# Kernel tuning notes

Measured on AMD Instinct MI355X. Metric: run time of the kernel, lower is better.

The kernel has to match this reference:

```python
import jax, jax.numpy as jnp
import numpy as np

# cfg dims: B batch, LQ max_que_len, O max_opt_count, LO max_opt_len,
# S max_sent_para, W max_words_sent, D word_emb
B, LQ, O, LO, S, W, D = 64, 64, 8, 32, 64, 32, 512
NEG_BIG = -9.0e15  # torch masked_fill constant for empty sentences


def setup_inputs() -> dict:
    key = jax.random.key(0)
    k1, k2, k3 = jax.random.split(key, 3)
    que_feat = jax.random.normal(k1, (B, LQ, D), dtype=jnp.float32)
    opt_feat = jax.random.normal(k2, (B, O, LO, D), dtype=jnp.float32)
    csf = jax.random.normal(k3, (B, S, W, D), dtype=jnp.float32)
    csf_mask = jnp.zeros((B, S, W), dtype=bool)   # True = padding word
    opt_sum = jnp.zeros((B, O), dtype=bool)       # True = empty option
    return dict(que_feat=que_feat, opt_feat=opt_feat, csf=csf,
                csf_mask=csf_mask, opt_sum=opt_sum)


def reference(que_feat, opt_feat, csf, csf_mask, opt_sum):
    b, s, w, d = csf.shape
    o = opt_feat.shape[1]

    # per-sentence valid length; empty sentences get a huge-magnitude divisor
    csf_len = jnp.sum(~csf_mask, axis=-1)                      # [B,S]
    csf_len = jnp.where(csf_len == 0, NEG_BIG,
                        csf_len.astype(jnp.float32))

    # question -> context sentence score: sum over query words and sentence
    # words of dot products (original: matmul + two sums, fused here)
    att_q2c = jnp.einsum('bqd,bswd->bs', que_feat, csf)        # [B,S]
    ix_q2c = jnp.argmax(att_q2c / csf_len, axis=-1)            # [B]

    # gather best sentence per batch item, broadcast over options
    que_csf = jnp.take_along_axis(
        csf, ix_q2c[:, None, None, None], axis=1)[:, 0]        # [B,W,D]
    que_csf = jnp.broadcast_to(que_csf[:, None], (b, o, w, d))
    que_csf = jnp.where(opt_sum[:, :, None, None], 0.0, que_csf)

    # option -> context sentence score
    att_o2c = jnp.einsum('bold,bswd->bos', opt_feat, csf)      # [B,O,S]
    ix_o2c = jnp.argmax(att_o2c / csf_len[:, None, :], axis=-1)  # [B,O]

    # faithful to original get_opt2csf: indexes csf[0] for EVERY batch item
    opt_csf = csf[0][ix_o2c]                                   # [B,O,W,D]
    opt_csf = jnp.where(opt_sum[:, :, None, None], 0.0, opt_csf)

    # make_mask: positions whose feature vector is all-zero
    que_csf_mask = jnp.sum(jnp.abs(que_csf), axis=-1) == 0     # [B,O,W]
    opt_csf_mask = jnp.sum(jnp.abs(opt_csf), axis=-1) == 0     # [B,O,W]
    return que_csf, que_csf_mask, opt_csf, opt_csf_mask
```

## Files before the change

### kernel.cpp

```cpp
#include <hip/hip_runtime.h>
#include <hip/hip_cooperative_groups.h>
#include <stddef.h>

namespace cg = cooperative_groups;

#define B  64
#define LQ 64
#define O  8
#define LO 32
#define S  64
#define W  32
#define D  512

#define NEG_BIG (-9.0e15f)

#define QUE_CSF_SZ  (B*O*W*D)
#define MASK_SZ     (B*O*W)
#define OFF_QMASK   (QUE_CSF_SZ)
#define OFF_OPT     (QUE_CSF_SZ + MASK_SZ)
#define OFF_OMASK   (QUE_CSF_SZ + MASK_SZ + QUE_CSF_SZ)

#define WS_QSUMH 0
#define WS_OSUM  (B*2*D)
#define WS_SC    (B*2*D + B*O*D)

#define NBLK 2368

using f4 = __attribute__((ext_vector_type(4))) float;

__device__ inline float dot4(f4 a, f4 b) {
  return a.x * b.x + a.y * b.y + a.z * b.z + a.w * b.w;
}

#define RED(v)                \
  do {                        \
    v += __shfl_xor(v, 32);   \
    v += __shfl_xor(v, 16);   \
    v += __shfl_xor(v, 8);    \
    v += __shfl_xor(v, 4);    \
    v += __shfl_xor(v, 2);    \
    v += __shfl_xor(v, 1);    \
  } while (0)

#define ARGMAX(v, idx)                                         \
  do {                                                         \
    for (int off_ = 32; off_; off_ >>= 1) {                    \
      float ov_ = __shfl_xor(v, off_);                         \
      int oi_ = __shfl_xor(idx, off_);                         \
      if (ov_ > v || (ov_ == v && oi_ < idx)) { v = ov_; idx = oi_; } \
    }                                                          \
  } while (0)

__device__ inline void dots9(const float* __restrict__ ws, f4 acc, int b,
                             int wv, int lane, float part[2][9]) {
  const f4* qh = (const f4*)(ws + WS_QSUMH) + (size_t)b * 256;
  const int t = wv * 64 + lane;
  f4 qs = qh[t] + qh[128 + t];
  float pq = dot4(acc, qs);
  float po[O];
  #pragma unroll
  for (int o = 0; o < O; ++o)
    po[o] = dot4(acc, ((const f4*)(ws + WS_OSUM))[((size_t)(b * O + o)) * 128 + t]);
  RED(pq);
  #pragma unroll
  for (int o = 0; o < O; ++o) RED(po[o]);
  if (lane == 0) {
    part[wv][0] = pq;
    #pragma unroll
    for (int o = 0; o < O; ++o) part[wv][1 + o] = po[o];
  }
}

__global__ __launch_bounds__(128, 5) void k_fused(
    const float* __restrict__ que, const float* __restrict__ opt,
    const float* __restrict__ csf, const unsigned char* __restrict__ csf_mask,
    const unsigned char* __restrict__ opt_sum, float* __restrict__ ws,
    float* __restrict__ out) {
  const int blk = blockIdx.x;
  const int t = threadIdx.x;
  const int wv = t >> 6;
  const int lane = t & 63;
  const int g1 = blk + NBLK;
  const bool j1csf = (g1 < 4096);

  const f4* p0 = (const f4*)csf + (size_t)blk * 4096 + t;
  const f4* p1;
  if (j1csf)            p1 = (const f4*)csf + (size_t)g1 * 4096 + t;
  else if (g1 < 4224)   p1 = (const f4*)que + (size_t)(g1 - 4096) * 4096 + t;
  else                  p1 = (const f4*)opt + (size_t)(g1 - 4224) * 4096 + t;

  f4 acc0 = {0.f, 0.f, 0.f, 0.f};
  f4 acc1 = {0.f, 0.f, 0.f, 0.f};
  #pragma unroll 8
  for (int r = 0; r < 32; ++r) {
    acc0 += p0[(size_t)r * 128];
    acc1 += p1[(size_t)r * 128];
  }
  if (!j1csf) {
    if (g1 < 4224)
      ((f4*)(ws + WS_QSUMH))[(size_t)(g1 - 4096) * 128 + t] = acc1;
    else
      ((f4*)(ws + WS_OSUM))[(size_t)(g1 - 4224) * 128 + t] = acc1;
  }

  __threadfence();
  cg::this_grid().sync();

  __shared__ float part[2][2][9];
  dots9(ws, acc0, blk >> 6, wv, lane, part[0]);
  if (j1csf) dots9(ws, acc1, g1 >> 6, wv, lane, part[1]);

  float len;
  {
    const int bs = (wv == 0) ? blk : g1;
    int pad = 0;
    if (lane < W && (wv == 0 || j1csf))
      pad = (csf_mask[(size_t)bs * W + lane] != 0) ? 1 : 0;
    const unsigned long long bal = __ballot(pad);
    const int valid = W - (int)__popcll(bal);
    len = (valid == 0) ? NEG_BIG : (float)valid;
  }
  __syncthreads();

  if (t < 9) {
    const int b0 = blk >> 6, s0 = blk & 63;
    ws[WS_SC + ((size_t)t * B + b0) * S + s0] =
        (part[0][0][t] + part[0][1][t]) / len;
  }
  if (j1csf && t >= 64 && t < 73) {
    const int q = t - 64;
    const int b1 = g1 >> 6, s1 = g1 & 63;
    ws[WS_SC + ((size_t)q * B + b1) * S + s1] =
        (part[1][0][q] + part[1][1][q]) / len;
  }

  __threadfence();
  cg::this_grid().sync();

  for (int row = blk * 2 + wv; row < B * O * W; row += NBLK * 2) {
    const int w = row & 31;
    const int bo = row >> 5;
    const int b = bo >> 3;
    const int o = bo & 7;

    float vq_ = ws[WS_SC + (size_t)b * S + lane];
    int iq = lane;
    ARGMAX(vq_, iq);
    float vo_ = ws[WS_SC + ((size_t)(1 + o) * B + b) * S + lane];
    int io = lane;
    ARGMAX(vo_, io);

    const bool zero = (opt_sum[bo] != 0);
    f4 a0 = {0.f, 0.f, 0.f, 0.f}, a1 = a0, b0 = a0, b1 = a0;
    if (!zero) {
      const f4* qrow = (const f4*)csf + (((size_t)b * S + iq) * W + w) * 128;
      a0 = qrow[lane];
      a1 = qrow[64 + lane];
      const f4* orow = (const f4*)csf + ((size_t)io * W + w) * 128;
      b0 = orow[lane];
      b1 = orow[64 + lane];
    }
    f4* oq = (f4*)(out + (size_t)row * D);
    f4* oo = (f4*)(out + OFF_OPT + (size_t)row * D);
    __builtin_nontemporal_store(a0, oq + lane);
    __builtin_nontemporal_store(a1, oq + 64 + lane);
    __builtin_nontemporal_store(b0, oo + lane);
    __builtin_nontemporal_store(b1, oo + 64 + lane);

    float aq = fabsf(a0.x) + fabsf(a0.y) + fabsf(a0.z) + fabsf(a0.w) +
               fabsf(a1.x) + fabsf(a1.y) + fabsf(a1.z) + fabsf(a1.w);
    float ao = fabsf(b0.x) + fabsf(b0.y) + fabsf(b0.z) + fabsf(b0.w) +
               fabsf(b1.x) + fabsf(b1.y) + fabsf(b1.z) + fabsf(b1.w);
    RED(aq);
    RED(ao);
    if (lane == 0) {
      out[OFF_QMASK + row] = (aq == 0.f) ? 1.f : 0.f;
      out[OFF_OMASK + row] = (ao == 0.f) ? 1.f : 0.f;
    }
  }
}

template <int ROWS>
__device__ inline void rowsum4(const f4* __restrict__ src, f4* __restrict__ dst,
                               int t) {
  const int quarter = t >> 7;
  const int col = t & 127;
  const f4* p = src + (size_t)(quarter * (ROWS / 4)) * 128 + col;
  f4 acc = {0.f, 0.f, 0.f, 0.f};
  #pragma unroll
  for (int r = 0; r < ROWS / 4; ++r) acc += p[(size_t)r * 128];
  __shared__ f4 tmp[3][128];
  if (quarter) tmp[quarter - 1][col] = acc;
  __syncthreads();
  if (quarter == 0) dst[col] = acc + tmp[0][col] + tmp[1][col] + tmp[2][col];
}

__global__ __launch_bounds__(512) void k_qosum(
    const float* __restrict__ que, const float* __restrict__ opt,
    float* __restrict__ ws) {
  const int blk = blockIdx.x;
  const int t = threadIdx.x;
  if (blk < B) {
    rowsum4<LQ>((const f4*)que + (size_t)blk * LQ * 128,
                (f4*)(ws + WS_QSUMH) + (size_t)blk * 256, t);
    if (t < 128) {
      f4 z = {0.f, 0.f, 0.f, 0.f};
      ((f4*)(ws + WS_QSUMH))[(size_t)blk * 256 + 128 + t] = z;
    }
  } else {
    const int bo = blk - B;
    rowsum4<LO>((const f4*)opt + (size_t)bo * LO * 128,
                (f4*)(ws + WS_OSUM) + (size_t)bo * 128, t);
  }
}

__global__ __launch_bounds__(128) void k_score(
    const float* __restrict__ csf, const unsigned char* __restrict__ csf_mask,
    float* __restrict__ ws) {
  const int bs = blockIdx.x;
  const int b = bs >> 6;
  const int s = bs & 63;
  const int t = threadIdx.x;
  const int wv = t >> 6;
  const int lane = t & 63;

  const f4* p = (const f4*)csf + (size_t)bs * 4096 + t;
  f4 acc = {0.f, 0.f, 0.f, 0.f};
  #pragma unroll 8
  for (int r = 0; r < 32; ++r) acc += p[(size_t)r * 128];

  __shared__ float part[2][9];
  dots9(ws, acc, b, wv, lane, part);

  int pad = 0;
  if (lane < W) pad = (csf_mask[(size_t)bs * W + lane] != 0) ? 1 : 0;
  const unsigned long long bal = __ballot(pad);
  const int valid = W - (int)__popcll(bal);
  const float len = (valid == 0) ? NEG_BIG : (float)valid;

  __syncthreads();
  if (t < 9)
    ws[WS_SC + ((size_t)t * B + b) * S + s] = (part[0][t] + part[1][t]) / len;
}

__global__ __launch_bounds__(128) void k_gather(
    const float* __restrict__ csf, const unsigned char* __restrict__ opt_sum,
    const float* __restrict__ ws, float* __restrict__ out) {
  const int bow = blockIdx.x;
  const int w = bow & 31;
  const int bo = bow >> 5;
  const int b = bo >> 3;
  const int o = bo & 7;
  const int t = threadIdx.x;
  const int wv = t >> 6;
  const int lane = t & 63;

  __shared__ int sh_ix[2];
  {
    const int q = (wv == 0) ? 0 : (1 + o);
    float v = ws[WS_SC + ((size_t)q * B + b) * S + lane];
    int idx = lane;
    ARGMAX(v, idx);
    if (lane == 0) sh_ix[wv] = idx;
  }
  __syncthreads();

  const bool zero = (opt_sum[bo] != 0);
  f4 vq = {0.f, 0.f, 0.f, 0.f};
  f4 vo = {0.f, 0.f, 0.f, 0.f};
  if (!zero) {
    const int iq = sh_ix[0];
    const int io = sh_ix[1];
    vq = ((const f4*)csf)[(((size_t)b * S + iq) * W + w) * 128 + t];
    vo = ((const f4*)csf)[((size_t)io * W + w) * 128 + t];
  }
  __builtin_nontemporal_store(vq, (f4*)(out + (size_t)bow * D) + t);
  __builtin_nontemporal_store(vo, (f4*)(out + OFF_OPT + (size_t)bow * D) + t);

  float aq = fabsf(vq.x) + fabsf(vq.y) + fabsf(vq.z) + fabsf(vq.w);
  float ao = fabsf(vo.x) + fabsf(vo.y) + fabsf(vo.z) + fabsf(vo.w);
  RED(aq);
  RED(ao);

  __shared__ float sq[2], so[2];
  if (lane == 0) { sq[wv] = aq; so[wv] = ao; }
  __syncthreads();
  if (t == 0) {
    out[OFF_QMASK + bow] = ((sq[0] + sq[1]) == 0.f) ? 1.f : 0.f;
    out[OFF_OMASK + bow] = ((so[0] + so[1]) == 0.f) ? 1.f : 0.f;
  }
}

extern "C" void kernel_launch(void* const* d_in, const int* in_sizes, int n_in,
                              void* d_out, int out_size, void* d_ws, size_t ws_size,
                              hipStream_t stream) {
  const float* que = (const float*)d_in[0];
  const float* opt = (const float*)d_in[1];
  const float* csf = (const float*)d_in[2];
  const unsigned char* csf_mask = (const unsigned char*)d_in[3];
  const unsigned char* opt_sum = (const unsigned char*)d_in[4];
  float* out = (float*)d_out;
  float* ws = (float*)d_ws;

  int coop = 0;
  {
    int dev = 0;
    hipDeviceProp_t prop{};
    int mb = 0;
    if (hipGetDevice(&dev) == hipSuccess &&
        hipGetDeviceProperties(&prop, dev) == hipSuccess &&
        hipOccupancyMaxActiveBlocksPerMultiprocessor(&mb, k_fused, 128, 0) ==
            hipSuccess) {
      if (prop.cooperativeLaunch &&
          (long)mb * prop.multiProcessorCount >= NBLK)
        coop = 1;
    }
  }

  if (coop) {
    void* args[] = {(void*)&que, (void*)&opt, (void*)&csf, (void*)&csf_mask,
                    (void*)&opt_sum, (void*)&ws, (void*)&out};
    if (hipLaunchCooperativeKernel(k_fused, dim3(NBLK), dim3(128), args, 0,
                                   stream) != hipSuccess)
      coop = 0;
  }
  if (!coop) {
    k_qosum<<<B + B * O, 512, 0, stream>>>(que, opt, ws);
    k_score<<<B * S, 128, 0, stream>>>(csf, csf_mask, ws);
    k_gather<<<B * O * W, 128, 0, stream>>>(csf, opt_sum, ws, out);
  }
}
```

Measured before the change: 70.59 us.

## Replace cooperative grid syncs with atomic-flag pipeline and dynamic chunk scheduling

Drops the cooperative launch and its two grid-wide barriers in favour of a regular launch of 2048 blocks. Blocks first compute the question and option sums and signal a counter, then pull sentence chunks from an atomic work queue, computing scores and bumping per-batch done counters. Each block then spins only on its own batch's counter before gathering 8 output rows. The intent is to overlap phases and replace full-grid barriers with finer-grained dependencies. It relies on all 2048 blocks being co-resident (assumes 256 CUs from the occupancy check), adds a memset launch, and risks deadlock or spin contention if residency fails.

```diff
diff --git a/kernel.cpp b/kernel.cpp
--- a/kernel.cpp
+++ b/kernel.cpp
@@ -1,8 +1,5 @@
 #include <hip/hip_runtime.h>
-#include <hip/hip_cooperative_groups.h>
 #include <stddef.h>
-
-namespace cg = cooperative_groups;
 
 #define B  64
 #define LQ 64
@@ -23,8 +20,12 @@
 #define WS_QSUMH 0
 #define WS_OSUM  (B*2*D)
 #define WS_SC    (B*2*D + B*O*D)
-
-#define NBLK 2368
+#define WS_FLAGS (WS_SC + 9*B*S)
+#define N_FLAGS  66
+
+#define NBLK      2048
+#define N_SUM     640
+#define N_CSF     4096
 
 using f4 = __attribute__((ext_vector_type(4))) float;
 
@@ -42,14 +43,21 @@
     v += __shfl_xor(v, 1);    \
   } while (0)
 
-#define ARGMAX(v, idx)                                         \
-  do {                                                         \
-    for (int off_ = 32; off_; off_ >>= 1) {                    \
-      float ov_ = __shfl_xor(v, off_);                         \
-      int oi_ = __shfl_xor(idx, off_);                         \
+#define ARGMAX(v, idx)                                                \
+  do {                                                                \
+    for (int off_ = 32; off_; off_ >>= 1) {                           \
+      float ov_ = __shfl_xor(v, off_);                                \
+      int oi_ = __shfl_xor(idx, off_);                                \
       if (ov_ > v || (ov_ == v && oi_ < idx)) { v = ov_; idx = oi_; } \
-    }                                                          \
+    }                                                                 \
   } while (0)
+
+__device__ inline f4 stream32(const f4* __restrict__ p, int t) {
+  f4 acc = {0.f, 0.f, 0.f, 0.f};
+  #pragma unroll 8
+  for (int r = 0; r < 32; ++r) acc += p[(size_t)r * 128 + t];
+  return acc;
+}
 
 __device__ inline void dots9(const float* __restrict__ ws, f4 acc, int b,
                              int wv, int lane, float part[2][9]) {
@@ -71,7 +79,17 @@
   }
 }
 
-__global__ __launch_bounds__(128, 5) void k_fused(
+__device__ inline void spin_until(int* p, int target) {
+  if (threadIdx.x == 0) {
+    while (__hip_atomic_load(p, __ATOMIC_ACQUIRE, __HIP_MEMORY_SCOPE_AGENT) <
+           target)
+      __builtin_amdgcn_s_sleep(8);
+  }
+  __syncthreads();
+  __threadfence();
+}
+
+__global__ __launch_bounds__(128, 4) void k_pipe(
     const float* __restrict__ que, const float* __restrict__ opt,
     const float* __restrict__ csf, const unsigned char* __restrict__ csf_mask,
     const unsigned char* __restrict__ opt_sum, float* __restrict__ ws,
@@ -80,68 +98,73 @@
   const int t = threadIdx.x;
   const int wv = t >> 6;
   const int lane = t & 63;
-  const int g1 = blk + NBLK;
-  const bool j1csf = (g1 < 4096);
-
-  const f4* p0 = (const f4*)csf + (size_t)blk * 4096 + t;
-  const f4* p1;
-  if (j1csf)            p1 = (const f4*)csf + (size_t)g1 * 4096 + t;
-  else if (g1 < 4224)   p1 = (const f4*)que + (size_t)(g1 - 4096) * 4096 + t;
-  else                  p1 = (const f4*)opt + (size_t)(g1 - 4224) * 4096 + t;
-
-  f4 acc0 = {0.f, 0.f, 0.f, 0.f};
-  f4 acc1 = {0.f, 0.f, 0.f, 0.f};
-  #pragma unroll 8
-  for (int r = 0; r < 32; ++r) {
-    acc0 += p0[(size_t)r * 128];
-    acc1 += p1[(size_t)r * 128];
-  }
-  if (!j1csf) {
-    if (g1 < 4224)
-      ((f4*)(ws + WS_QSUMH))[(size_t)(g1 - 4096) * 128 + t] = acc1;
-    else
-      ((f4*)(ws + WS_OSUM))[(size_t)(g1 - 4224) * 128 + t] = acc1;
-  }
-
-  __threadfence();
-  cg::this_grid().sync();
-
-  __shared__ float part[2][2][9];
-  dots9(ws, acc0, blk >> 6, wv, lane, part[0]);
-  if (j1csf) dots9(ws, acc1, g1 >> 6, wv, lane, part[1]);
-
-  float len;
-  {
-    const int bs = (wv == 0) ? blk : g1;
+
+  int* flags = (int*)(ws + WS_FLAGS);
+  int* done_sum = flags;
+  int* next_chunk = flags + 1;
+  int* done_score = flags + 2;
+
+  if (blk < N_SUM) {
+    f4 acc;
+    if (blk < 128) {
+      acc = stream32((const f4*)que + (size_t)blk * 4096, t);
+      ((f4*)(ws + WS_QSUMH))[(size_t)blk * 128 + t] = acc;
+    } else {
+      const int bo = blk - 128;
+      acc = stream32((const f4*)opt + (size_t)bo * 4096, t);
+      ((f4*)(ws + WS_OSUM))[(size_t)bo * 128 + t] = acc;
+    }
+    __syncthreads();
+    if (t == 0) {
+      __threadfence();
+      __hip_atomic_fetch_add(done_sum, 1, __ATOMIC_RELEASE,
+                             __HIP_MEMORY_SCOPE_AGENT);
+    }
+  }
+
+  __shared__ int sh_c;
+  __shared__ float part[2][9];
+  bool waited = false;
+  for (;;) {
+    if (t == 0) sh_c = atomicAdd(next_chunk, 1);
+    __syncthreads();
+    const int c = sh_c;
+    __syncthreads();
+    if (c >= N_CSF) break;
+    const int b = c >> 6, s = c & 63;
+
+    f4 acc = stream32((const f4*)csf + (size_t)c * 4096, t);
+
+    if (!waited) {
+      spin_until(done_sum, N_SUM);
+      waited = true;
+    }
+
+    dots9(ws, acc, b, wv, lane, part);
+
     int pad = 0;
-    if (lane < W && (wv == 0 || j1csf))
-      pad = (csf_mask[(size_t)bs * W + lane] != 0) ? 1 : 0;
+    if (lane < W) pad = (csf_mask[(size_t)c * W + lane] != 0) ? 1 : 0;
     const unsigned long long bal = __ballot(pad);
     const int valid = W - (int)__popcll(bal);
-    len = (valid == 0) ? NEG_BIG : (float)valid;
-  }
-  __syncthreads();
-
-  if (t < 9) {
-    const int b0 = blk >> 6, s0 = blk & 63;
-    ws[WS_SC + ((size_t)t * B + b0) * S + s0] =
-        (part[0][0][t] + part[0][1][t]) / len;
-  }
-  if (j1csf && t >= 64 && t < 73) {
-    const int q = t - 64;
-    const int b1 = g1 >> 6, s1 = g1 & 63;
-    ws[WS_SC + ((size_t)q * B + b1) * S + s1] =
-        (part[1][0][q] + part[1][1][q]) / len;
-  }
-
-  __threadfence();
-  cg::this_grid().sync();
-
-  for (int row = blk * 2 + wv; row < B * O * W; row += NBLK * 2) {
-    const int w = row & 31;
-    const int bo = row >> 5;
-    const int b = bo >> 3;
-    const int o = bo & 7;
+    const float len = (valid == 0) ? NEG_BIG : (float)valid;
+
+    __syncthreads();
+    if (t < 9)
+      ws[WS_SC + ((size_t)t * B + b) * S + s] = (part[0][t] + part[1][t]) / len;
+    __syncthreads();
+    if (t == 0) {
+      __threadfence();
+      __hip_atomic_fetch_add(&done_score[b], 1, __ATOMIC_RELEASE,
+                             __HIP_MEMORY_SCOPE_AGENT);
+    }
+  }
+
+  {
+    const int b = blk >> 5;
+    const int o = (blk >> 2) & 7;
+    const int w0 = (blk & 3) * 8;
+
+    spin_until(&done_score[b], S);
 
     float vq_ = ws[WS_SC + (size_t)b * S + lane];
     int iq = lane;
@@ -150,32 +173,39 @@
     int io = lane;
     ARGMAX(vo_, io);
 
-    const bool zero = (opt_sum[bo] != 0);
-    f4 a0 = {0.f, 0.f, 0.f, 0.f}, a1 = a0, b0 = a0, b1 = a0;
-    if (!zero) {
-      const f4* qrow = (const f4*)csf + (((size_t)b * S + iq) * W + w) * 128;
-      a0 = qrow[lane];
-      a1 = qrow[64 + lane];
-      const f4* orow = (const f4*)csf + ((size_t)io * W + w) * 128;
-      b0 = orow[lane];
-      b1 = orow[64 + lane];
-    }
-    f4* oq = (f4*)(out + (size_t)row * D);
-    f4* oo = (f4*)(out + OFF_OPT + (size_t)row * D);
-    __builtin_nontemporal_store(a0, oq + lane);
-    __builtin_nontemporal_store(a1, oq + 64 + lane);
-    __builtin_nontemporal_store(b0, oo + lane);
-    __builtin_nontemporal_store(b1, oo + 64 + lane);
-
-    float aq = fabsf(a0.x) + fabsf(a0.y) + fabsf(a0.z) + fabsf(a0.w) +
-               fabsf(a1.x) + fabsf(a1.y) + fabsf(a1.z) + fabsf(a1.w);
-    float ao = fabsf(b0.x) + fabsf(b0.y) + fabsf(b0.z) + fabsf(b0.w) +
-               fabsf(b1.x) + fabsf(b1.y) + fabsf(b1.z) + fabsf(b1.w);
-    RED(aq);
-    RED(ao);
-    if (lane == 0) {
-      out[OFF_QMASK + row] = (aq == 0.f) ? 1.f : 0.f;
-      out[OFF_OMASK + row] = (ao == 0.f) ? 1.f : 0.f;
+    const bool zero = (opt_sum[b * O + o] != 0);
+    const f4* qbase = (const f4*)csf + ((size_t)b * S + iq) * W * 128;
+    const f4* obase = (const f4*)csf + (size_t)io * W * 128;
+
+    #pragma unroll
+    for (int i = 0; i < 4; ++i) {
+      const int w = w0 + wv * 4 + i;
+      const int row = (b * O + o) * W + w;
+
+      f4 a0 = {0.f, 0.f, 0.f, 0.f}, a1 = a0, b0 = a0, b1 = a0;
+      if (!zero) {
+        a0 = qbase[(size_t)w * 128 + lane];
+        a1 = qbase[(size_t)w * 128 + 64 + lane];
+        b0 = obase[(size_t)w * 128 + lane];
+        b1 = obase[(size_t)w * 128 + 64 + lane];
+      }
+      f4* oq = (f4*)(out + (size_t)row * D);
+      f4* oo = (f4*)(out + OFF_OPT + (size_t)row * D);
+      __builtin_nontemporal_store(a0, oq + lane);
+      __builtin_nontemporal_store(a1, oq + 64 + lane);
+      __builtin_nontemporal_store(b0, oo + lane);
+      __builtin_nontemporal_store(b1, oo + 64 + lane);
+
+      float aq = fabsf(a0.x) + fabsf(a0.y) + fabsf(a0.z) + fabsf(a0.w) +
+                 fabsf(a1.x) + fabsf(a1.y) + fabsf(a1.z) + fabsf(a1.w);
+      float ao = fabsf(b0.x) + fabsf(b0.y) + fabsf(b0.z) + fabsf(b0.w) +
+                 fabsf(b1.x) + fabsf(b1.y) + fabsf(b1.z) + fabsf(b1.w);
+      RED(aq);
+      RED(ao);
+      if (lane == 0) {
+        out[OFF_QMASK + row] = (aq == 0.f) ? 1.f : 0.f;
+        out[OFF_OMASK + row] = (ao == 0.f) ? 1.f : 0.f;
+      }
     }
   }
 }
@@ -224,10 +254,7 @@
   const int wv = t >> 6;
   const int lane = t & 63;
 
-  const f4* p = (const f4*)csf + (size_t)bs * 4096 + t;
-  f4 acc = {0.f, 0.f, 0.f, 0.f};
-  #pragma unroll 8
-  for (int r = 0; r < 32; ++r) acc += p[(size_t)r * 128];
+  f4 acc = stream32((const f4*)csf + (size_t)bs * 4096, t);
 
   __shared__ float part[2][9];
   dots9(ws, acc, b, wv, lane, part);
@@ -302,29 +329,19 @@
   float* out = (float*)d_out;
   float* ws = (float*)d_ws;
 
-  int coop = 0;
+  int ok = 0;
   {
-    int dev = 0;
-    hipDeviceProp_t prop{};
     int mb = 0;
-    if (hipGetDevice(&dev) == hipSuccess &&
-        hipGetDeviceProperties(&prop, dev) == hipSuccess &&
-        hipOccupancyMaxActiveBlocksPerMultiprocessor(&mb, k_fused, 128, 0) ==
-            hipSuccess) {
-      if (prop.cooperativeLaunch &&
-          (long)mb * prop.multiProcessorCount >= NBLK)
-        coop = 1;
-    }
-  }
-
-  if (coop) {
-    void* args[] = {(void*)&que, (void*)&opt, (void*)&csf, (void*)&csf_mask,
-                    (void*)&opt_sum, (void*)&ws, (void*)&out};
-    if (hipLaunchCooperativeKernel(k_fused, dim3(NBLK), dim3(128), args, 0,
-                                   stream) != hipSuccess)
-      coop = 0;
-  }
-  if (!coop) {
+    if (hipOccupancyMaxActiveBlocksPerMultiprocessor(&mb, k_pipe, 128, 0) ==
+            hipSuccess &&
+        mb >= NBLK / 256)
+      ok = 1;
+  }
+
+  if (ok) {
+    hipMemsetAsync(ws + WS_FLAGS, 0, N_FLAGS * sizeof(int), stream);
+    k_pipe<<<NBLK, 128, 0, stream>>>(que, opt, csf, csf_mask, opt_sum, ws, out);
+  } else {
     k_qosum<<<B + B * O, 512, 0, stream>>>(que, opt, ws);
     k_score<<<B * S, 128, 0, stream>>>(csf, csf_mask, ws);
     k_gather<<<B * O * W, 128, 0, stream>>>(csf, opt_sum, ws, out);
```

Result: no change. 70.39 us (-0.3%).
